# Optimization experiments

Measured on AMD Instinct MI355X. Metric: run time of the kernel, lower is better.

Reference implementation:

```python
import jax, jax.numpy as jnp
import numpy as np

ROUTINGS = 3

def squash(s, axis=-1):
    # drives long vectors toward length 1, short vectors toward 0
    norm = jnp.linalg.norm(s, axis=axis, keepdims=True)
    scale = norm ** 2 / (1.0 + norm ** 2) / (norm + 1e-8)
    return scale * s

def dense_capsule(x, W, routings=ROUTINGS):
    # x: [B, I, Di], W: [O, I, Do, Di] -> out: [B, O, Do]
    # torch.matmul(W, x[:,None,:,:,None]).squeeze(-1) == einsum over Di
    x_hat = jnp.einsum('oidc,bic->boid', W, x)          # [B, O, I, Do]
    x_hat_det = jax.lax.stop_gradient(x_hat)
    B, O, I, _ = x_hat.shape
    b = jnp.zeros((B, O, I), dtype=x_hat.dtype)
    outputs = None
    for i in range(routings):
        c = jax.nn.softmax(b, axis=1)                    # [B, O, I]
        if i == routings - 1:
            outputs = squash(jnp.sum(c[..., None] * x_hat, axis=2, keepdims=True))
        else:
            outputs = squash(jnp.sum(c[..., None] * x_hat_det, axis=2, keepdims=True))
            b = b + jnp.sum(outputs * x_hat_det, axis=-1)
    return jnp.squeeze(outputs, axis=2)                  # [B, O, Do]

INIT_NUM_CAP = 128
INIT_DIM_CAP = 8

def setup_inputs() -> dict:
    key = jax.random.key(0)
    k0, k1, k2, k3 = jax.random.split(key, 4)
    x = jax.random.normal(k0, (1024, 1024), dtype=jnp.float32)
    W0 = 0.01 * jax.random.normal(k1, (64, 128, 16, 8), dtype=jnp.float32)
    W1 = 0.01 * jax.random.normal(k2, (32, 64, 32, 16), dtype=jnp.float32)
    W2 = 0.01 * jax.random.normal(k3, (10, 32, 64, 32), dtype=jnp.float32)
    return {"x": x, "W0": W0, "W1": W1, "W2": W2}

def reference(x, W0, W1, W2):
    h = x.reshape(-1, INIT_NUM_CAP, INIT_DIM_CAP)        # [B, 128, 8]
    for W in (W0, W1, W2):
        h = dense_capsule(h, W)
    return jnp.linalg.norm(h, axis=-1)                   # [B, 10]
```

## Files before the change

### kernel.cpp

```cpp
#include <hip/hip_runtime.h>
#include <math.h>

typedef unsigned int u32;

__device__ __forceinline__ u32 pk2(float a, float b){
    u32 ua=__float_as_uint(a), ub=__float_as_uint(b);
    u32 ra=(ua + 0x7fffu + ((ua>>16)&1u))>>16;
    u32 rb=(ub + 0x7fffu + ((ub>>16)&1u))>>16;
    return ra | (rb<<16);
}
__device__ __forceinline__ float lo16(u32 p){ return __uint_as_float(p<<16); }
__device__ __forceinline__ float hi16(u32 p){ return __uint_as_float(p & 0xffff0000u); }

#if __has_builtin(__builtin_amdgcn_fdot2_f32_bf16)
__device__ __forceinline__ float dot2bf(u32 a, u32 b, float c){
    float d;
    asm("v_dot2_f32_bf16 %0, %1, %2, %3" : "=v"(d) : "v"(a), "v"(b), "v"(c));
    return d;
}
#else
__device__ __forceinline__ float dot2bf(u32 a, u32 b, float c){
    return fmaf(hi16(a), hi16(b), fmaf(lo16(a), lo16(b), c));
}
#endif

__device__ __forceinline__ void gll16(const u32* gp, u32* lp){
    __builtin_amdgcn_global_load_lds((const __attribute__((address_space(1))) void*)gp,
                                     (__attribute__((address_space(3))) void*)lp,
                                     16, 0, 0);
}

template<int I,int Di,int O,int Do,int IR>
__global__ void k_conv(const float* __restrict__ W, u32* __restrict__ Wb){
    constexpr int CB=Di/8, LPO=Do/16, GR=LPO*O, NSL=16*CB;
    const int n = O*I*Do*Di/2;
    for (int t = blockIdx.x*blockDim.x+threadIdx.x; t < n; t += gridDim.x*blockDim.x){
        int cw = t & 3;
        int u4 = t >> 2;
        int g    = u4 % GR;  int r1 = u4 / GR;
        int slot = r1 % NSL; int r2 = r1 / NSL;
        int il   = r2 % IR;  int si = r2 / IR;
        int i  = si*IR + il;
        int j  = slot / CB, cb = slot % CB;
        int o  = g % O,     q  = g / O;
        int jg = q*16 + j;
        int c  = cb*8 + cw*2;
        const float* src = W + ((size_t)(o*I + i)*Do + jg)*Di + c;
        Wb[t] = pk2(src[0], src[1]);
    }
}

template<int I,int Di,int O,int Do,int IR,int ES,bool LOGIT,bool XS>
__global__ __launch_bounds__(512,1) void k_contract(
    const u32* __restrict__ Wb, const void* __restrict__ hsrc,
    const u32* __restrict__ vsb, u32* __restrict__ ps)
{
    constexpr int CB=Di/8, LPO=Do/16, ACT=O*LPO, GR=LPO*O, NSL=16*CB;
    constexpr int SLICE  = IR*NSL*GR*4;
    constexpr int ROUNDS = SLICE/2048;
    __shared__ __align__(16) u32 slab[SLICE];

    const int tid = threadIdx.x;
    const int w = tid>>6, l = tid&63;
    const int eg = blockIdx.x, si = blockIdx.y;

    {
        const u32* g = Wb + (size_t)si*SLICE + tid*4;
        u32* ld = slab + w*256;
        #pragma unroll
        for (int rd=0; rd<ROUNDS; ++rd) gll16(g + rd*2048, ld + rd*2048);
    }
    __syncthreads();

    const bool act = l < ACT;
    const int qL = act ? (l%LPO) : 0;
    const int oL = act ? (l/LPO) : 0;
    const int lnoff = qL*O + oL;
    const uint4* W4 = (const uint4*)slab;

    for (int ee=0; ee<8/ES; ++ee){
        const int e0 = eg*64 + w*8 + ee*ES;

        u32 vp[ES][8];
        if constexpr (LOGIT){
            #pragma unroll
            for (int k=0;k<ES;++k){
                uint4 a = *(const uint4*)(vsb + (size_t)(e0+k)*512 + l*8);
                uint4 b = *(const uint4*)(vsb + (size_t)(e0+k)*512 + l*8 + 4);
                vp[k][0]=a.x; vp[k][1]=a.y; vp[k][2]=a.z; vp[k][3]=a.w;
                vp[k][4]=b.x; vp[k][5]=b.y; vp[k][6]=b.z; vp[k][7]=b.w;
            }
        }

        float sacc[ES][16];
        #pragma unroll
        for (int k=0;k<ES;++k)
            #pragma unroll
            for (int j=0;j<16;++j) sacc[k][j]=0.f;

        for (int il=0; il<IR; ++il){
            u32 hk[ES][Di/2];
            if constexpr (XS){
                #pragma unroll
                for (int k=0;k<ES;++k){
                    const float* xp = (const float*)hsrc + (size_t)(e0+k)*1024 + (si*IR+il)*Di;
                    #pragma unroll
                    for (int f4=0; f4<Di/4; ++f4){
                        float4 f = *(const float4*)(xp + 4*f4);
                        hk[k][2*f4+0] = pk2(f.x, f.y);
                        hk[k][2*f4+1] = pk2(f.z, f.w);
                    }
                }
            } else {
                #pragma unroll
                for (int k=0;k<ES;++k){
                    const u32* hp = (const u32*)hsrc + (size_t)(e0+k)*512 + (si*IR+il)*(Di/2);
                    #pragma unroll
                    for (int t4=0; t4<Di/8; ++t4){
                        uint4 hv = *(const uint4*)(hp + 4*t4);
                        hk[k][4*t4+0]=hv.x; hk[k][4*t4+1]=hv.y;
                        hk[k][4*t4+2]=hv.z; hk[k][4*t4+3]=hv.w;
                    }
                }
            }

            float xh[ES][16];
            #pragma unroll
            for (int k=0;k<ES;++k)
                #pragma unroll
                for (int j=0;j<16;++j) xh[k][j]=0.f;

            #pragma unroll
            for (int j=0;j<16;++j)
                #pragma unroll
                for (int cb=0;cb<CB;++cb){
                    uint4 wv = W4[(il*NSL + j*CB + cb)*GR + lnoff];
                    #pragma unroll
                    for (int k=0;k<ES;++k){
                        float t = xh[k][j];
                        t = dot2bf(wv.x, hk[k][cb*4+0], t);
                        t = dot2bf(wv.y, hk[k][cb*4+1], t);
                        t = dot2bf(wv.z, hk[k][cb*4+2], t);
                        t = dot2bf(wv.w, hk[k][cb*4+3], t);
                        xh[k][j] = t;
                    }
                }

            float cc[ES];
            if constexpr (!LOGIT){
                #pragma unroll
                for (int k=0;k<ES;++k) cc[k]=1.f;
            } else {
                #pragma unroll
                for (int k=0;k<ES;++k){
                    float lp=0.f;
                    #pragma unroll
                    for (int jj=0;jj<8;++jj)
                        lp += lo16(vp[k][jj])*xh[k][2*jj] + hi16(vp[k][jj])*xh[k][2*jj+1];
                    if constexpr (LPO>=2) lp += __shfl_xor(lp,1,64);
                    if constexpr (LPO>=4) lp += __shfl_xor(lp,2,64);
                    float ev = act ? __expf(lp) : 0.f;
                    float tot = ev;
                    tot+=__shfl_xor(tot,1,64);  tot+=__shfl_xor(tot,2,64);
                    tot+=__shfl_xor(tot,4,64);  tot+=__shfl_xor(tot,8,64);
                    tot+=__shfl_xor(tot,16,64); tot+=__shfl_xor(tot,32,64);
                    cc[k] = ev*(float)LPO/tot;
                }
            }
            #pragma unroll
            for (int k=0;k<ES;++k)
                #pragma unroll
                for (int j=0;j<16;++j) sacc[k][j] += cc[k]*xh[k][j];
        }

        if (act){
            #pragma unroll
            for (int k=0;k<ES;++k){
                u32* pp = ps + ((size_t)(si*1024 + e0 + k))*512 + l*8;
                uint4 o0, o1;
                o0.x=pk2(sacc[k][0],sacc[k][1]);   o0.y=pk2(sacc[k][2],sacc[k][3]);
                o0.z=pk2(sacc[k][4],sacc[k][5]);   o0.w=pk2(sacc[k][6],sacc[k][7]);
                o1.x=pk2(sacc[k][8],sacc[k][9]);   o1.y=pk2(sacc[k][10],sacc[k][11]);
                o1.z=pk2(sacc[k][12],sacc[k][13]); o1.w=pk2(sacc[k][14],sacc[k][15]);
                *(uint4*)pp = o0;
                *(uint4*)(pp+4) = o1;
            }
        }
    }
}

template<int O,int Do,int MODE>
__global__ __launch_bounds__(256) void k_squash(
    const u32* __restrict__ ps, u32* __restrict__ vsb, void* __restrict__ dst)
{
    constexpr int LPO=Do/16, ACT=O*LPO;
    const int tid=threadIdx.x, w=tid>>6, l=tid&63;
    const int e = blockIdx.x*4 + w;
    const bool act = l < ACT;
    const int oL = act ? (l/LPO) : 0;

    float s[16];
    #pragma unroll
    for (int j=0;j<16;++j) s[j]=0.f;
    #pragma unroll
    for (int si=0; si<16; ++si){
        const u32* pp = ps + ((size_t)(si*1024 + e))*512 + l*8;
        uint4 a = *(const uint4*)pp;
        uint4 b = *(const uint4*)(pp+4);
        u32 q[8] = {a.x,a.y,a.z,a.w,b.x,b.y,b.z,b.w};
        #pragma unroll
        for (int k=0;k<8;++k){ s[2*k] += lo16(q[k]); s[2*k+1] += hi16(q[k]); }
    }
    if constexpr (MODE==0){
        #pragma unroll
        for (int j=0;j<16;++j) s[j] *= (1.0f/(float)O);
    }
    float n2=0.f;
    #pragma unroll
    for (int j=0;j<16;++j) n2 += s[j]*s[j];
    if constexpr (LPO>=2) n2 += __shfl_xor(n2,1,64);
    if constexpr (LPO>=4) n2 += __shfl_xor(n2,2,64);
    float nrm   = sqrtf(n2);
    float scale = n2/((1.f+n2)*(nrm+1e-8f));

    if constexpr (MODE==0){
        if (act){
            u32* vp = vsb + (size_t)e*512 + l*8;
            #pragma unroll
            for (int k=0;k<8;++k) vp[k] = pk2(scale*s[2*k], scale*s[2*k+1]);
        }
    } else if constexpr (MODE==1){
        if (act){
            u32* vp = vsb + (size_t)e*512 + l*8;
            #pragma unroll
            for (int k=0;k<8;++k){
                u32 old = vp[k];
                vp[k] = pk2(lo16(old)+scale*s[2*k], hi16(old)+scale*s[2*k+1]);
            }
        }
    } else if constexpr (MODE==2){
        if (act){
            u32* hp = (u32*)dst + (size_t)e*512 + l*8;
            #pragma unroll
            for (int k=0;k<8;++k) hp[k] = pk2(scale*s[2*k], scale*s[2*k+1]);
        }
    } else {
        float q=0.f;
        #pragma unroll
        for (int j=0;j<16;++j){ float vj=scale*s[j]; q += vj*vj; }
        if constexpr (LPO>=2) q += __shfl_xor(q,1,64);
        if constexpr (LPO>=4) q += __shfl_xor(q,2,64);
        if (act && (l%LPO)==0)
            ((float*)dst)[(size_t)e*O + oL] = sqrtf(q);
    }
}

template<int I, int Di, int O, int Do, bool FINAL>
__device__ __forceinline__ void fb_layer(const float* __restrict__ W, float* __restrict__ hl,
                                         float* __restrict__ out, int e, int l) {
    constexpr int LPO = Do / 16;
    constexpr int ACT = O * LPO;
    const int o  = l / LPO;
    const int d0 = (l % LPO) * 16;
    const bool act = (l < ACT);
    float vs[16];
    #pragma unroll
    for (int j = 0; j < 16; ++j) vs[j] = 0.f;
    for (int r = 0; r < 3; ++r) {
        float sacc[16];
        #pragma unroll
        for (int j = 0; j < 16; ++j) sacc[j] = 0.f;
        for (int i = 0; i < I; ++i) {
            if ((i & 15) == 0) __syncthreads();
            float xh[16];
            #pragma unroll
            for (int j = 0; j < 16; ++j) xh[j] = 0.f;
            if (act) {
                const float* wb = W + ((size_t)(o * I + i) * Do + d0) * Di;
                #pragma unroll
                for (int j = 0; j < 16; ++j) {
                    const float4* wr = (const float4*)(wb + j * Di);
                    float acc = 0.f;
                    #pragma unroll
                    for (int c4 = 0; c4 < Di / 4; ++c4) {
                        float4 wv = wr[c4];
                        float4 hv = *(const float4*)(hl + i * Di + c4 * 4);
                        acc += wv.x*hv.x + wv.y*hv.y + wv.z*hv.z + wv.w*hv.w;
                    }
                    xh[j] = acc;
                }
            }
            float cc;
            if (r == 0) cc = 1.0f;
            else {
                float lp = 0.f;
                #pragma unroll
                for (int j = 0; j < 16; ++j) lp += vs[j] * xh[j];
                if constexpr (LPO >= 2) lp += __shfl_xor(lp, 1, 64);
                if constexpr (LPO >= 4) lp += __shfl_xor(lp, 2, 64);
                float ev = act ? __expf(lp) : 0.f;
                float tot = ev;
                tot += __shfl_xor(tot,1,64); tot += __shfl_xor(tot,2,64);
                tot += __shfl_xor(tot,4,64); tot += __shfl_xor(tot,8,64);
                tot += __shfl_xor(tot,16,64); tot += __shfl_xor(tot,32,64);
                cc = ev * (float)LPO / tot;
            }
            #pragma unroll
            for (int j = 0; j < 16; ++j) sacc[j] += cc * xh[j];
        }
        if (r == 0) {
            #pragma unroll
            for (int j = 0; j < 16; ++j) sacc[j] *= (1.0f / O);
        }
        float n2 = 0.f;
        #pragma unroll
        for (int j = 0; j < 16; ++j) n2 += sacc[j] * sacc[j];
        if constexpr (LPO >= 2) n2 += __shfl_xor(n2, 1, 64);
        if constexpr (LPO >= 4) n2 += __shfl_xor(n2, 2, 64);
        float nrm = sqrtf(n2);
        float scale = n2 / ((1.f + n2) * (nrm + 1e-8f));
        if (r < 2) {
            #pragma unroll
            for (int j = 0; j < 16; ++j) vs[j] += scale * sacc[j];
        } else {
            if constexpr (FINAL) {
                float q = 0.f;
                #pragma unroll
                for (int j = 0; j < 16; ++j) { float vj = scale*sacc[j]; q += vj*vj; }
                if constexpr (LPO >= 2) q += __shfl_xor(q, 1, 64);
                if constexpr (LPO >= 4) q += __shfl_xor(q, 2, 64);
                if (act && (l % LPO) == 0) out[(size_t)e * O + o] = sqrtf(q);
            } else {
                __syncthreads();
                if (act) {
                    #pragma unroll
                    for (int j = 0; j < 16; ++j) hl[o * Do + d0 + j] = scale * sacc[j];
                }
                __syncthreads();
            }
        }
    }
}

__global__ __launch_bounds__(256) void fb_caps(const float* __restrict__ x,
                                               const float* __restrict__ W0,
                                               const float* __restrict__ W1,
                                               const float* __restrict__ W2,
                                               float* __restrict__ out) {
    __shared__ float hsh[4][1024];
    const int w = threadIdx.x >> 6;
    const int l = threadIdx.x & 63;
    const int e = blockIdx.x * 4 + w;
    float* hl = hsh[w];
    const float4* xr = (const float4*)(x + (size_t)e * 1024);
    float4* h4 = (float4*)hl;
    #pragma unroll
    for (int k = 0; k < 4; ++k) h4[l + 64 * k] = xr[l + 64 * k];
    __syncthreads();
    fb_layer<128, 8, 64, 16, false>(W0, hl, out, e, l);
    fb_layer<64, 16, 32, 32, false>(W1, hl, out, e, l);
    fb_layer<32, 32, 10, 64, true >(W2, hl, out, e, l);
}

extern "C" void kernel_launch(void* const* d_in, const int* in_sizes, int n_in,
                              void* d_out, int out_size, void* d_ws, size_t ws_size,
                              hipStream_t stream) {
    const float* x  = (const float*)d_in[0];
    const float* W0 = (const float*)d_in[1];
    const float* W1 = (const float*)d_in[2];
    const float* W2 = (const float*)d_in[3];
    float* out = (float*)d_out;

    const size_t DW0 = 524288, DW1 = 524288, DW2 = 327680;
    const size_t DPS = (size_t)16*1024*512;
    const size_t DVS = (size_t)1024*512;
    const size_t DH  = (size_t)1024*512;
    const size_t need = (DW0+DW1+DW2+DPS+DVS+2*DH)*4;

    if (ws_size < need) {
        fb_caps<<<256, 256, 0, stream>>>(x, W0, W1, W2, out);
        return;
    }

    u32* Wb0 = (u32*)d_ws;
    u32* Wb1 = Wb0 + DW0;
    u32* Wb2 = Wb1 + DW1;
    u32* ps  = Wb2 + DW2;
    u32* vs  = ps  + DPS;
    u32* h1  = vs  + DVS;
    u32* h2  = h1  + DH;

    k_conv<128, 8,64,16,8><<<256,256,0,stream>>>(W0, Wb0);
    k_conv< 64,16,32,32,4><<<256,256,0,stream>>>(W1, Wb1);
    k_conv< 32,32,10,64,2><<<256,256,0,stream>>>(W2, Wb2);

    dim3 g(16,16);

    k_contract<128,8,64,16,8,4,false,true ><<<g,512,0,stream>>>(Wb0, x, vs, ps);
    k_squash<64,16,0><<<256,256,0,stream>>>(ps, vs, nullptr);
    k_contract<128,8,64,16,8,4,true ,true ><<<g,512,0,stream>>>(Wb0, x, vs, ps);
    k_squash<64,16,1><<<256,256,0,stream>>>(ps, vs, nullptr);
    k_contract<128,8,64,16,8,4,true ,true ><<<g,512,0,stream>>>(Wb0, x, vs, ps);
    k_squash<64,16,2><<<256,256,0,stream>>>(ps, vs, h1);

    k_contract<64,16,32,32,4,4,false,false><<<g,512,0,stream>>>(Wb1, h1, vs, ps);
    k_squash<32,32,0><<<256,256,0,stream>>>(ps, vs, nullptr);
    k_contract<64,16,32,32,4,4,true ,false><<<g,512,0,stream>>>(Wb1, h1, vs, ps);
    k_squash<32,32,1><<<256,256,0,stream>>>(ps, vs, nullptr);
    k_contract<64,16,32,32,4,4,true ,false><<<g,512,0,stream>>>(Wb1, h1, vs, ps);
    k_squash<32,32,2><<<256,256,0,stream>>>(ps, vs, h2);

    k_contract<32,32,10,64,2,2,false,false><<<g,512,0,stream>>>(Wb2, h2, vs, ps);
    k_squash<10,64,0><<<256,256,0,stream>>>(ps, vs, nullptr);
    k_contract<32,32,10,64,2,2,true ,false><<<g,512,0,stream>>>(Wb2, h2, vs, ps);
    k_squash<10,64,1><<<256,256,0,stream>>>(ps, vs, nullptr);
    k_contract<32,32,10,64,2,2,true ,false><<<g,512,0,stream>>>(Wb2, h2, vs, ps);
    k_squash<10,64,3><<<256,256,0,stream>>>(ps, vs, out);
}
```

Before: 477.6 us.

## Halve LDS weight slab to allow two blocks per CU and pre-pack input

The contract kernel now stages the weight slice into LDS in two halves instead of all at once. That halves shared memory per block, so launch bounds can allow two blocks per CU, and the grid doubles to 32x16 with 4 samples per wave instead of 8. A separate pack kernel converts x to bf16 once, so the first-layer contractions no longer repeat the float-to-bf16 conversion. Layer outputs now reuse a single h buffer. In exchange, each block restages weights once per sample group and adds extra barriers, and the doubled grid means twice as many total weight loads.

```diff
diff --git a/kernel.cpp b/kernel.cpp
--- a/kernel.cpp
+++ b/kernel.cpp
@@ -50,27 +50,31 @@
     }
 }
 
-template<int I,int Di,int O,int Do,int IR,int ES,bool LOGIT,bool XS>
-__global__ __launch_bounds__(512,1) void k_contract(
-    const u32* __restrict__ Wb, const void* __restrict__ hsrc,
+__global__ void k_pack(const float* __restrict__ x, u32* __restrict__ hb){
+    int t = blockIdx.x*blockDim.x + threadIdx.x;
+    if (t < 1024*512){
+        float2 f = ((const float2*)x)[t];
+        hb[t] = pk2(f.x, f.y);
+    }
+}
+
+template<int I,int Di,int O,int Do,int IR,int ES,bool LOGIT>
+__global__ __launch_bounds__(512,2) void k_contract(
+    const u32* __restrict__ Wb, const u32* __restrict__ hsrc,
     const u32* __restrict__ vsb, u32* __restrict__ ps)
 {
     constexpr int CB=Di/8, LPO=Do/16, ACT=O*LPO, GR=LPO*O, NSL=16*CB;
-    constexpr int SLICE  = IR*NSL*GR*4;
-    constexpr int ROUNDS = SLICE/2048;
-    __shared__ __align__(16) u32 slab[SLICE];
+    constexpr int SLICE = IR*NSL*GR*4;
+    constexpr int HALF  = SLICE/2;
+    constexpr int IRH   = IR/2;
+    constexpr int ROUNDS = HALF/2048;
+    static_assert(HALF % 2048 == 0, "staging granularity");
+    static_assert(HALF <= 16384, "64KB slab");
+    __shared__ __align__(16) u32 slab[HALF];
 
     const int tid = threadIdx.x;
     const int w = tid>>6, l = tid&63;
     const int eg = blockIdx.x, si = blockIdx.y;
-
-    {
-        const u32* g = Wb + (size_t)si*SLICE + tid*4;
-        u32* ld = slab + w*256;
-        #pragma unroll
-        for (int rd=0; rd<ROUNDS; ++rd) gll16(g + rd*2048, ld + rd*2048);
-    }
-    __syncthreads();
 
     const bool act = l < ACT;
     const int qL = act ? (l%LPO) : 0;
@@ -78,8 +82,16 @@
     const int lnoff = qL*O + oL;
     const uint4* W4 = (const uint4*)slab;
 
-    for (int ee=0; ee<8/ES; ++ee){
-        const int e0 = eg*64 + w*8 + ee*ES;
+    auto stage = [&](int ch){
+        const u32* g = Wb + (size_t)si*SLICE + ch*HALF + tid*4;
+        u32* ld = slab + w*256;
+        #pragma unroll
+        for (int rd=0; rd<ROUNDS; ++rd) gll16(g + rd*2048, ld + rd*2048);
+    };
+
+    bool first = true;
+    for (int ee=0; ee<4/ES; ++ee){
+        const int e0 = eg*32 + w*4 + ee*ES;
 
         u32 vp[ES][8];
         if constexpr (LOGIT){
@@ -98,23 +110,20 @@
             #pragma unroll
             for (int j=0;j<16;++j) sacc[k][j]=0.f;
 
-        for (int il=0; il<IR; ++il){
-            u32 hk[ES][Di/2];
-            if constexpr (XS){
+        for (int ch=0; ch<2; ++ch){
+            if (!first) __syncthreads();
+            first = false;
+            stage(ch);
+            __syncthreads();
+
+            #pragma unroll
+            for (int il2=0; il2<IRH; ++il2){
+                const int i = si*IR + ch*IRH + il2;
+
+                u32 hk[ES][Di/2];
                 #pragma unroll
                 for (int k=0;k<ES;++k){
-                    const float* xp = (const float*)hsrc + (size_t)(e0+k)*1024 + (si*IR+il)*Di;
-                    #pragma unroll
-                    for (int f4=0; f4<Di/4; ++f4){
-                        float4 f = *(const float4*)(xp + 4*f4);
-                        hk[k][2*f4+0] = pk2(f.x, f.y);
-                        hk[k][2*f4+1] = pk2(f.z, f.w);
-                    }
-                }
-            } else {
-                #pragma unroll
-                for (int k=0;k<ES;++k){
-                    const u32* hp = (const u32*)hsrc + (size_t)(e0+k)*512 + (si*IR+il)*(Di/2);
+                    const u32* hp = hsrc + (size_t)(e0+k)*512 + i*(Di/2);
                     #pragma unroll
                     for (int t4=0; t4<Di/8; ++t4){
                         uint4 hv = *(const uint4*)(hp + 4*t4);
@@ -122,55 +131,55 @@
                         hk[k][4*t4+2]=hv.z; hk[k][4*t4+3]=hv.w;
                     }
                 }
-            }
-
-            float xh[ES][16];
-            #pragma unroll
-            for (int k=0;k<ES;++k)
-                #pragma unroll
-                for (int j=0;j<16;++j) xh[k][j]=0.f;
-
-            #pragma unroll
-            for (int j=0;j<16;++j)
-                #pragma unroll
-                for (int cb=0;cb<CB;++cb){
-                    uint4 wv = W4[(il*NSL + j*CB + cb)*GR + lnoff];
+
+                float xh[ES][16];
+                #pragma unroll
+                for (int k=0;k<ES;++k)
+                    #pragma unroll
+                    for (int j=0;j<16;++j) xh[k][j]=0.f;
+
+                #pragma unroll
+                for (int j=0;j<16;++j)
+                    #pragma unroll
+                    for (int cb=0;cb<CB;++cb){
+                        uint4 wv = W4[(il2*NSL + j*CB + cb)*GR + lnoff];
+                        #pragma unroll
+                        for (int k=0;k<ES;++k){
+                            float t = xh[k][j];
+                            t = dot2bf(wv.x, hk[k][cb*4+0], t);
+                            t = dot2bf(wv.y, hk[k][cb*4+1], t);
+                            t = dot2bf(wv.z, hk[k][cb*4+2], t);
+                            t = dot2bf(wv.w, hk[k][cb*4+3], t);
+                            xh[k][j] = t;
+                        }
+                    }
+
+                float cc[ES];
+                if constexpr (!LOGIT){
+                    #pragma unroll
+                    for (int k=0;k<ES;++k) cc[k]=1.f;
+                } else {
                     #pragma unroll
                     for (int k=0;k<ES;++k){
-                        float t = xh[k][j];
-                        t = dot2bf(wv.x, hk[k][cb*4+0], t);
-                        t = dot2bf(wv.y, hk[k][cb*4+1], t);
-                        t = dot2bf(wv.z, hk[k][cb*4+2], t);
-                        t = dot2bf(wv.w, hk[k][cb*4+3], t);
-                        xh[k][j] = t;
+                        float lp=0.f;
+                        #pragma unroll
+                        for (int jj=0;jj<8;++jj)
+                            lp += lo16(vp[k][jj])*xh[k][2*jj] + hi16(vp[k][jj])*xh[k][2*jj+1];
+                        if constexpr (LPO>=2) lp += __shfl_xor(lp,1,64);
+                        if constexpr (LPO>=4) lp += __shfl_xor(lp,2,64);
+                        float ev = act ? __expf(lp) : 0.f;
+                        float tot = ev;
+                        tot+=__shfl_xor(tot,1,64);  tot+=__shfl_xor(tot,2,64);
+                        tot+=__shfl_xor(tot,4,64);  tot+=__shfl_xor(tot,8,64);
+                        tot+=__shfl_xor(tot,16,64); tot+=__shfl_xor(tot,32,64);
+                        cc[k] = ev*(float)LPO/tot;
                     }
                 }
-
-            float cc[ES];
-            if constexpr (!LOGIT){
-                #pragma unroll
-                for (int k=0;k<ES;++k) cc[k]=1.f;
-            } else {
-                #pragma unroll
-                for (int k=0;k<ES;++k){
-                    float lp=0.f;
-                    #pragma unroll
-                    for (int jj=0;jj<8;++jj)
-                        lp += lo16(vp[k][jj])*xh[k][2*jj] + hi16(vp[k][jj])*xh[k][2*jj+1];
-                    if constexpr (LPO>=2) lp += __shfl_xor(lp,1,64);
-                    if constexpr (LPO>=4) lp += __shfl_xor(lp,2,64);
-                    float ev = act ? __expf(lp) : 0.f;
-                    float tot = ev;
-                    tot+=__shfl_xor(tot,1,64);  tot+=__shfl_xor(tot,2,64);
-                    tot+=__shfl_xor(tot,4,64);  tot+=__shfl_xor(tot,8,64);
-                    tot+=__shfl_xor(tot,16,64); tot+=__shfl_xor(tot,32,64);
-                    cc[k] = ev*(float)LPO/tot;
-                }
-            }
-            #pragma unroll
-            for (int k=0;k<ES;++k)
-                #pragma unroll
-                for (int j=0;j<16;++j) sacc[k][j] += cc[k]*xh[k][j];
+                #pragma unroll
+                for (int k=0;k<ES;++k)
+                    #pragma unroll
+                    for (int j=0;j<16;++j) sacc[k][j] += cc[k]*xh[k][j];
+            }
         }
 
         if (act){
@@ -375,7 +384,7 @@
     const size_t DPS = (size_t)16*1024*512;
     const size_t DVS = (size_t)1024*512;
     const size_t DH  = (size_t)1024*512;
-    const size_t need = (DW0+DW1+DW2+DPS+DVS+2*DH)*4;
+    const size_t need = (DW0+DW1+DW2+DPS+DVS+DH)*4;
 
     if (ws_size < need) {
         fb_caps<<<256, 256, 0, stream>>>(x, W0, W1, W2, out);
@@ -387,33 +396,33 @@
     u32* Wb2 = Wb1 + DW1;
     u32* ps  = Wb2 + DW2;
     u32* vs  = ps  + DPS;
-    u32* h1  = vs  + DVS;
-    u32* h2  = h1  + DH;
+    u32* hb  = vs  + DVS;
 
     k_conv<128, 8,64,16,8><<<256,256,0,stream>>>(W0, Wb0);
     k_conv< 64,16,32,32,4><<<256,256,0,stream>>>(W1, Wb1);
     k_conv< 32,32,10,64,2><<<256,256,0,stream>>>(W2, Wb2);
-
-    dim3 g(16,16);
-
-    k_contract<128,8,64,16,8,4,false,true ><<<g,512,0,stream>>>(Wb0, x, vs, ps);
+    k_pack<<<1024,512,0,stream>>>(x, hb);
+
+    dim3 g(32,16);
+
+    k_contract<128,8,64,16,8,4,false><<<g,512,0,stream>>>(Wb0, hb, vs, ps);
     k_squash<64,16,0><<<256,256,0,stream>>>(ps, vs, nullptr);
-    k_contract<128,8,64,16,8,4,true ,true ><<<g,512,0,stream>>>(Wb0, x, vs, ps);
+    k_contract<128,8,64,16,8,4,true ><<<g,512,0,stream>>>(Wb0, hb, vs, ps);
     k_squash<64,16,1><<<256,256,0,stream>>>(ps, vs, nullptr);
-    k_contract<128,8,64,16,8,4,true ,true ><<<g,512,0,stream>>>(Wb0, x, vs, ps);
-    k_squash<64,16,2><<<256,256,0,stream>>>(ps, vs, h1);
-
-    k_contract<64,16,32,32,4,4,false,false><<<g,512,0,stream>>>(Wb1, h1, vs, ps);
+    k_contract<128,8,64,16,8,4,true ><<<g,512,0,stream>>>(Wb0, hb, vs, ps);
+    k_squash<64,16,2><<<256,256,0,stream>>>(ps, vs, hb);
+
+    k_contract<64,16,32,32,4,4,false><<<g,512,0,stream>>>(Wb1, hb, vs, ps);
     k_squash<32,32,0><<<256,256,0,stream>>>(ps, vs, nullptr);
-    k_contract<64,16,32,32,4,4,true ,false><<<g,512,0,stream>>>(Wb1, h1, vs, ps);
+    k_contract<64,16,32,32,4,4,true ><<<g,512,0,stream>>>(Wb1, hb, vs, ps);
     k_squash<32,32,1><<<256,256,0,stream>>>(ps, vs, nullptr);
-    k_contract<64,16,32,32,4,4,true ,false><<<g,512,0,stream>>>(Wb1, h1, vs, ps);
-    k_squash<32,32,2><<<256,256,0,stream>>>(ps, vs, h2);
-
-    k_contract<32,32,10,64,2,2,false,false><<<g,512,0,stream>>>(Wb2, h2, vs, ps);
+    k_contract<64,16,32,32,4,4,true ><<<g,512,0,stream>>>(Wb1, hb, vs, ps);
+    k_squash<32,32,2><<<256,256,0,stream>>>(ps, vs, hb);
+
+    k_contract<32,32,10,64,2,2,false><<<g,512,0,stream>>>(Wb2, hb, vs, ps);
     k_squash<10,64,0><<<256,256,0,stream>>>(ps, vs, nullptr);
-    k_contract<32,32,10,64,2,2,true ,false><<<g,512,0,stream>>>(Wb2, h2, vs, ps);
+    k_contract<32,32,10,64,2,2,true ><<<g,512,0,stream>>>(Wb2, hb, vs, ps);
     k_squash<10,64,1><<<256,256,0,stream>>>(ps, vs, nullptr);
-    k_contract<32,32,10,64,2,2,true ,false><<<g,512,0,stream>>>(Wb2, h2, vs, ps);
+    k_contract<32,32,10,64,2,2,true ><<<g,512,0,stream>>>(Wb2, hb, vs, ps);
     k_squash<10,64,3><<<256,256,0,stream>>>(ps, vs, out);
 }
```

Result: slower. 762.5 us (+59.6%).
